# Performance work log

Hardware: AMD Instinct MI355X
Metric: run time of the kernel (lower is better)

## Reference

```python
import jax, jax.numpy as jnp
import numpy as np

B, S, D = 2, 2048, 2048
H, G = 32, 8            # n_heads, n_kv_groups
HD = D // H             # head_dim = 64
GS = H // G             # group_size = 4


def _rope(t, cos, sin):
    # t: (B, h, S, HD); cos/sin: (S, HD), start_pos = 0
    half = t.shape[-1] // 2
    rot = jnp.concatenate([-t[..., half:], t[..., :half]], axis=-1)
    return t * cos[None, None] + rot * sin[None, None]


def setup_inputs() -> dict:
    key = jax.random.key(0)
    ks = jax.random.split(key, 7)
    x = jax.random.normal(ks[0], (B, S, D), jnp.float32)
    cos = jax.random.normal(ks[1], (S, HD), jnp.float32)
    sin = jax.random.normal(ks[2], (S, HD), jnp.float32)
    mask = jnp.zeros((S, S), jnp.bool_)
    Wq = jax.random.normal(ks[3], (D, D), jnp.float32) * 0.02
    Wk = jax.random.normal(ks[4], (G * HD, D), jnp.float32) * 0.02
    Wv = jax.random.normal(ks[5], (G * HD, D), jnp.float32) * 0.02
    Wo = jax.random.normal(ks[6], (D, D), jnp.float32) * 0.02
    return {"x": x, "cos": cos, "sin": sin, "mask": mask,
            "Wq": Wq, "Wk": Wk, "Wv": Wv, "Wo": Wo}


def reference(x, cos, sin, mask, Wq, Wk, Wv, Wo):
    b, s, d = x.shape
    # projections (nn.Linear: y = x @ W.T)
    q = (x @ Wq.T).reshape(b, s, H, HD).transpose(0, 2, 1, 3)   # (b,H,s,HD)
    k = (x @ Wk.T).reshape(b, s, G, HD).transpose(0, 2, 1, 3)   # (b,G,s,HD)
    v = (x @ Wv.T).reshape(b, s, G, HD).transpose(0, 2, 1, 3)   # (b,G,s,HD)
    q = _rope(q, cos, sin)
    k = _rope(k, cos, sin)
    # GQA: heads grouped contiguously per kv group (equivalent to repeat_interleave on kv)
    qg = q.reshape(b, G, GS, s, HD)
    scores = jnp.einsum('bgmsd,bgtd->bgmst', qg, k) / jnp.sqrt(jnp.float32(HD))
    # NOTE: original calls non-inplace masked_fill and DISCARDS the result,
    # so the mask has no effect on the output; reproduced faithfully.
    attn = jax.nn.softmax(scores, axis=-1)
    y = jnp.einsum('bgmst,bgtd->bgmsd', attn, v)
    y = y.reshape(b, H, s, HD).transpose(0, 2, 1, 3).reshape(b, s, d)
    return y @ Wo.T
```

## Files before the change

### kernel.cpp

```cpp
#include <hip/hip_runtime.h>
#include <hip/hip_bf16.h>
#include <stdint.h>

#define B_ 2
#define S_ 2048
#define D_ 2048
#define H_ 32
#define G_ 8
#define HD_ 64
#define KVD (G_*HD_)

typedef unsigned short u16;
typedef unsigned int u32;
typedef __attribute__((ext_vector_type(8))) short s8v;
typedef __attribute__((ext_vector_type(4))) float f4v;
typedef __attribute__((ext_vector_type(4))) unsigned int u4v;

static __device__ __forceinline__ float bf2f(u16 u){ return __uint_as_float(((u32)u)<<16); }
static __device__ __forceinline__ u16 f2bf(float f){
  u32 b = __float_as_uint(f);
  return (u16)((b + 0x7FFFu + ((b>>16)&1u)) >> 16);
}
static __device__ __forceinline__ u32 pk2bf(float a, float b){
  float2 f2 = make_float2(a, b);
  __hip_bfloat162 h = __float22bfloat162_rn(f2);
  return *(u32*)&h;
}

struct CvtArgs {
  const float *x, *wq, *wk, *wv, *wo;
  u16 *xb, *wqkvb, *wob;
};
__global__ void k_cvt5(CvtArgs a){
  const int E0 = 2097152;
  const int E1 = E0 + 1048576;
  const int E2 = E1 + 262144;
  const int E3 = E2 + 262144;
  const int E4 = E3 + 1048576;
  int u = blockIdx.x*blockDim.x + threadIdx.x;
  int stride = gridDim.x*blockDim.x;
  for (; u < E4; u += stride){
    const float* s; u16* d; int off;
    if      (u < E0){ s = a.x;  d = a.xb;               off = u; }
    else if (u < E1){ s = a.wq; d = a.wqkvb;            off = u - E0; }
    else if (u < E2){ s = a.wk; d = a.wqkvb + 4194304;  off = u - E1; }
    else if (u < E3){ s = a.wv; d = a.wqkvb + 5242880;  off = u - E2; }
    else            { s = a.wo; d = a.wob;              off = u - E3; }
    float4 f = *(const float4*)(s + (long)off*4);
    uint2 o;
    o.x = (u32)f2bf(f.x) | ((u32)f2bf(f.y)<<16);
    o.y = (u32)f2bf(f.z) | ((u32)f2bf(f.w)<<16);
    *(uint2*)(d + (long)off*4) = o;
  }
}

template<int MODE>
__global__ __launch_bounds__(512) void k_gemm(const u16* __restrict__ A,
    const u16* __restrict__ Bw,
    void* __restrict__ C, void* __restrict__ C2, void* __restrict__ C3,
    const float* __restrict__ cs, const float* __restrict__ sn,
    int N_unused, int K){
  __shared__ u16 As[2][128*32];
  __shared__ u16 Bs[2][128*32];
  const int tid = threadIdx.x;
  const int lane = tid & 63, wid = tid >> 6;
  const int l15 = lane & 15, l4 = lane >> 4;
  const int wr = wid >> 1, wc = wid & 1;
  const long Arow0 = (long)blockIdx.x * 128;
  const long Brow0 = (long)blockIdx.y * 128;
  const int NKS = K >> 5;

  const int sc = tid;
  const int srow = sc >> 2, slot = sc & 3;
  const int ko = slot ^ (srow & 3);
  const u16* srcA0 = A  + (Arow0 + srow)*K + ko*8;
  const u16* srcB0 = Bw + (Brow0 + srow)*K + ko*8;
  auto stage = [&](int ks){
    int bsel = ks & 1, k0 = ks << 5;
    __builtin_amdgcn_global_load_lds(
        (__attribute__((address_space(1))) void*)(void*)(srcA0 + k0),
        (__attribute__((address_space(3))) void*)(&As[bsel][wid*512]), 16, 0, 0);
    __builtin_amdgcn_global_load_lds(
        (__attribute__((address_space(1))) void*)(void*)(srcB0 + k0),
        (__attribute__((address_space(3))) void*)(&Bs[bsel][wid*512]), 16, 0, 0);
  };

  f4v acc[2][4] = {};
  stage(0);
  for (int ks = 0; ks < NKS; ++ks){
    __syncthreads();
    if (ks + 1 < NKS) stage(ks + 1);
    const u16* AsB = As[ks & 1];
    const u16* BsB = Bs[ks & 1];
    s8v af[2], bf[4];
    #pragma unroll
    for (int m = 0; m < 2; ++m){
      int row = wr*32 + m*16 + l15;
      af[m] = *(const s8v*)((const char*)AsB + row*64 + ((l4 ^ (row & 3))<<4));
    }
    #pragma unroll
    for (int n = 0; n < 4; ++n){
      int col = wc*64 + n*16 + l15;
      bf[n] = *(const s8v*)((const char*)BsB + col*64 + ((l4 ^ (col & 3))<<4));
    }
    __builtin_amdgcn_s_setprio(1);
    #pragma unroll
    for (int m = 0; m < 2; ++m)
      #pragma unroll
      for (int n = 0; n < 4; ++n)
        acc[m][n] = __builtin_amdgcn_mfma_f32_16x16x32_bf16(af[m], bf[n], acc[m][n], 0, 0, 0);
    __builtin_amdgcn_s_setprio(0);
  }

  if (MODE == 0){
    #pragma unroll
    for (int m = 0; m < 2; ++m)
      #pragma unroll
      for (int n = 0; n < 4; ++n)
        #pragma unroll
        for (int i = 0; i < 4; ++i){
          long r = Arow0 + wr*32 + m*16 + l4*4 + i;
          long c = Brow0 + wc*64 + n*16 + l15;
          ((float*)C)[r*2048 + c] = acc[m][n][i];
        }
  } else {
    const long col0 = Brow0 + wc*64;
    if (col0 < 2560){
      u16* out; long cbase; int stride; float qs;
      if (col0 < 2048){ out = (u16*)C;  cbase = col0;        stride = 2048; qs = 0.125f*1.44269504f; }
      else            { out = (u16*)C2; cbase = col0 - 2048; stride = 512;  qs = 1.0f; }
      #pragma unroll
      for (int m = 0; m < 2; ++m){
        long r0 = Arow0 + wr*32 + m*16 + l4*4;
        #pragma unroll
        for (int i = 0; i < 4; ++i){
          int s = (int)((r0 + i) & (S_-1));
          const float* cb = cs + s*64 + l15;
          const float* sb = sn + s*64 + l15;
          #pragma unroll
          for (int n = 0; n < 2; ++n){
            float c0 = cb[n*16],      s0v = sb[n*16];
            float c1 = cb[n*16 + 32], s1v = sb[n*16 + 32];
            float t0 = acc[m][n][i], t1 = acc[m][n+2][i];
            long cA = cbase + n*16 + l15;
            out[(r0+i)*stride + cA]      = f2bf((t0*c0 - t1*s0v)*qs);
            out[(r0+i)*stride + cA + 32] = f2bf((t1*c1 + t0*s1v)*qs);
          }
        }
      }
    } else {
      u16* vt = (u16*)C3;
      int g = (int)((col0 - 2560) >> 6);
      #pragma unroll
      for (int m = 0; m < 2; ++m){
        long r0 = Arow0 + wr*32 + m*16 + l4*4;
        int b = (int)(r0 >> 11), s0 = (int)(r0 & (S_-1));
        #pragma unroll
        for (int n = 0; n < 4; ++n){
          int d = n*16 + l15;
          uint2 w;
          w.x = (u32)f2bf(acc[m][n][0]) | ((u32)f2bf(acc[m][n][1])<<16);
          w.y = (u32)f2bf(acc[m][n][2]) | ((u32)f2bf(acc[m][n][3])<<16);
          *(uint2*)(vt + ((long)(b*G_ + g)*64 + d)*S_ + s0) = w;
        }
      }
    }
  }
}

__global__ __launch_bounds__(512) void k_fattn(const u16* __restrict__ q,
    const u16* __restrict__ k, const u16* __restrict__ vt, u16* __restrict__ o){
  __shared__ u16 Ks[2][64*64];
  __shared__ u16 VTs[2][64*64];
  __shared__ u16 Ps[8][32*64];
  const int tid = threadIdx.x, lane = tid & 63, wid = tid >> 6;
  const int l15 = lane & 15, l4 = lane >> 4;
  const int qt = blockIdx.x, h = blockIdx.y, b = blockIdx.z;
  const int g = h >> 2;
  const long qrow0 = (long)b*S_ + qt*256 + wid*32;

  s8v aq[2][2];
  #pragma unroll
  for (int mf = 0; mf < 2; ++mf)
    #pragma unroll
    for (int kf = 0; kf < 2; ++kf)
      aq[mf][kf] = *(const s8v*)(q + (qrow0 + mf*16 + l15)*D_ + h*64 + kf*32 + l4*8);

  u4v ov; ov.x = ov.y = ov.z = ov.w = 0x3F803F80u;
  const s8v ones = *(s8v*)&ov;

  const int c = wid*64 + lane;
  const int srow = c >> 3, ko = (c & 7) ^ (srow & 7);
  const u16* ksrc0 = k  + ((long)b*S_ + srow)*KVD + g*64 + ko*8;
  const u16* vsrc0 = vt + ((long)(b*G_ + g)*64 + srow)*S_ + ko*8;

  auto stage = [&](int kt){
    int bsel = kt & 1;
    __builtin_amdgcn_global_load_lds(
        (__attribute__((address_space(1))) void*)(void*)(ksrc0 + (long)kt*64*KVD),
        (__attribute__((address_space(3))) void*)(&Ks[bsel][wid*512]), 16, 0, 0);
    __builtin_amdgcn_global_load_lds(
        (__attribute__((address_space(1))) void*)(void*)(vsrc0 + kt*64),
        (__attribute__((address_space(3))) void*)(&VTs[bsel][wid*512]), 16, 0, 0);
  };

  f4v oacc[2][4] = {};
  f4v lsacc[2] = {};

  stage(0);
  for (int kt = 0; kt < S_/64; ++kt){
    __syncthreads();
    if (kt + 1 < S_/64) stage(kt + 1);
    const u16* KsB = Ks[kt & 1];
    const u16* VsB = VTs[kt & 1];

    s8v bk[4][2];
    #pragma unroll
    for (int nf = 0; nf < 4; ++nf){
      int key = nf*16 + l15;
      #pragma unroll
      for (int kf = 0; kf < 2; ++kf)
        bk[nf][kf] = *(const s8v*)((const char*)KsB + key*128 + (((kf*4 + l4) ^ (key & 7))<<4));
    }
    f4v sacc[2][4] = {};
    __builtin_amdgcn_s_setprio(1);
    #pragma unroll
    for (int mf = 0; mf < 2; ++mf)
      #pragma unroll
      for (int nf = 0; nf < 4; ++nf)
        #pragma unroll
        for (int kf = 0; kf < 2; ++kf)
          sacc[mf][nf] = __builtin_amdgcn_mfma_f32_16x16x32_bf16(bk[nf][kf], aq[mf][kf], sacc[mf][nf], 0, 0, 0);
    __builtin_amdgcn_s_setprio(0);

    #pragma unroll
    for (int mf = 0; mf < 2; ++mf){
      int r = mf*16 + l15;
      char* pbase = (char*)Ps[wid] + r*128 + (l4 & 1)*8;
      #pragma unroll
      for (int nf = 0; nf < 4; ++nf){
        float p0 = __builtin_amdgcn_exp2f(sacc[mf][nf][0]);
        float p1 = __builtin_amdgcn_exp2f(sacc[mf][nf][1]);
        float p2 = __builtin_amdgcn_exp2f(sacc[mf][nf][2]);
        float p3 = __builtin_amdgcn_exp2f(sacc[mf][nf][3]);
        uint2 w; w.x = pk2bf(p0, p1); w.y = pk2bf(p2, p3);
        int slot = nf*2 + (l4 >> 1);
        *(uint2*)(pbase + ((slot ^ (r & 7))<<4)) = w;
      }
    }

    s8v ap[2][2];
    #pragma unroll
    for (int mf = 0; mf < 2; ++mf){
      int r = mf*16 + l15;
      #pragma unroll
      for (int kf = 0; kf < 2; ++kf)
        ap[mf][kf] = *(const s8v*)((const char*)Ps[wid] + r*128 + (((kf*4 + l4) ^ (r & 7))<<4));
    }
    __builtin_amdgcn_s_setprio(1);
    #pragma unroll
    for (int mf = 0; mf < 2; ++mf)
      #pragma unroll
      for (int kf = 0; kf < 2; ++kf)
        lsacc[mf] = __builtin_amdgcn_mfma_f32_16x16x32_bf16(ap[mf][kf], ones, lsacc[mf], 0, 0, 0);
    #pragma unroll
    for (int nd = 0; nd < 4; ++nd){
      int d = nd*16 + l15;
      #pragma unroll
      for (int kf = 0; kf < 2; ++kf){
        s8v bv = *(const s8v*)((const char*)VsB + d*128 + (((kf*4 + l4) ^ (d & 7))<<4));
        #pragma unroll
        for (int mf = 0; mf < 2; ++mf)
          oacc[mf][nd] = __builtin_amdgcn_mfma_f32_16x16x32_bf16(ap[mf][kf], bv, oacc[mf][nd], 0, 0, 0);
      }
    }
    __builtin_amdgcn_s_setprio(0);
  }

  #pragma unroll
  for (int mf = 0; mf < 2; ++mf){
    f4v li;
    #pragma unroll
    for (int i = 0; i < 4; ++i) li[i] = 1.f / lsacc[mf][i];
    #pragma unroll
    for (int nd = 0; nd < 4; ++nd){
      long r = qrow0 + mf*16 + l4*4;
      int cc = h*64 + nd*16 + l15;
      o[(r+0)*D_ + cc] = f2bf(oacc[mf][nd][0]*li[0]);
      o[(r+1)*D_ + cc] = f2bf(oacc[mf][nd][1]*li[1]);
      o[(r+2)*D_ + cc] = f2bf(oacc[mf][nd][2]*li[2]);
      o[(r+3)*D_ + cc] = f2bf(oacc[mf][nd][3]*li[3]);
    }
  }
}

extern "C" void kernel_launch(void* const* d_in, const int* in_sizes, int n_in,
                              void* d_out, int out_size, void* d_ws, size_t ws_size,
                              hipStream_t stream){
  const float* x    = (const float*)d_in[0];
  const float* cosp = (const float*)d_in[1];
  const float* sinp = (const float*)d_in[2];
  const float* Wq = (const float*)d_in[4];
  const float* Wk = (const float*)d_in[5];
  const float* Wv = (const float*)d_in[6];
  const float* Wo = (const float*)d_in[7];

  char* ws = (char*)d_ws;
  size_t off = 0;
  auto alloc = [&](size_t bytes)->char*{
    char* p = ws + off; off += (bytes + 255) & ~(size_t)255; return p;
  };
  u16* xb    = (u16*)alloc((size_t)8388608*2);
  u16* wqkvb = (u16*)alloc((size_t)6291456*2);
  u16* wob   = (u16*)alloc((size_t)4194304*2);
  u16* qb    = (u16*)alloc((size_t)8388608*2);
  u16* kb    = (u16*)alloc((size_t)2097152*2);
  u16* vtb   = (u16*)alloc((size_t)2097152*2);
  u16* ab    = (u16*)alloc((size_t)8388608*2);
  if (ws_size < off) return;

  CvtArgs ca{ x, Wq, Wk, Wv, Wo, xb, wqkvb, wob };
  k_cvt5<<<2048,256,0,stream>>>(ca);

  k_gemm<3><<<dim3(32,24,1),512,0,stream>>>(xb, wqkvb, qb, kb, vtb, cosp, sinp, 3072, 2048);

  k_fattn<<<dim3(8,32,2),512,0,stream>>>(qb, kb, vtb, ab);

  k_gemm<0><<<dim3(32,16,1),512,0,stream>>>(ab, wob, d_out, nullptr, nullptr, nullptr, nullptr, 2048, 2048);
}
```

Before: 206.9 us.

## Single-buffer K/V tiles in flash attention, raise occupancy, remap block order

```diff
diff --git a/kernel.cpp b/kernel.cpp
--- a/kernel.cpp
+++ b/kernel.cpp
@@ -168,14 +168,17 @@
   }
 }
 
-__global__ __launch_bounds__(512) void k_fattn(const u16* __restrict__ q,
+__global__ __launch_bounds__(512,6) void k_fattn(const u16* __restrict__ q,
     const u16* __restrict__ k, const u16* __restrict__ vt, u16* __restrict__ o){
-  __shared__ u16 Ks[2][64*64];
-  __shared__ u16 VTs[2][64*64];
+  __shared__ u16 Ks[64*64];
+  __shared__ u16 VTs[64*64];
   __shared__ u16 Ps[8][32*64];
   const int tid = threadIdx.x, lane = tid & 63, wid = tid >> 6;
   const int l15 = lane & 15, l4 = lane >> 4;
-  const int qt = blockIdx.x, h = blockIdx.y, b = blockIdx.z;
+  const int fid = blockIdx.x;
+  const int G = (fid >> 6)*8 + (fid & 7);
+  const int qt = (fid >> 3) & 7;
+  const int h = G & 31, b = G >> 5;
   const int g = h >> 2;
   const long qrow0 = (long)b*S_ + qt*256 + wid*32;
 
@@ -194,25 +197,17 @@
   const u16* ksrc0 = k  + ((long)b*S_ + srow)*KVD + g*64 + ko*8;
   const u16* vsrc0 = vt + ((long)(b*G_ + g)*64 + srow)*S_ + ko*8;
 
-  auto stage = [&](int kt){
-    int bsel = kt & 1;
+  f4v oacc[2][4] = {};
+  f4v lsacc[2] = {};
+
+  for (int kt = 0; kt < S_/64; ++kt){
     __builtin_amdgcn_global_load_lds(
         (__attribute__((address_space(1))) void*)(void*)(ksrc0 + (long)kt*64*KVD),
-        (__attribute__((address_space(3))) void*)(&Ks[bsel][wid*512]), 16, 0, 0);
+        (__attribute__((address_space(3))) void*)(&Ks[wid*512]), 16, 0, 0);
     __builtin_amdgcn_global_load_lds(
         (__attribute__((address_space(1))) void*)(void*)(vsrc0 + kt*64),
-        (__attribute__((address_space(3))) void*)(&VTs[bsel][wid*512]), 16, 0, 0);
-  };
-
-  f4v oacc[2][4] = {};
-  f4v lsacc[2] = {};
-
-  stage(0);
-  for (int kt = 0; kt < S_/64; ++kt){
+        (__attribute__((address_space(3))) void*)(&VTs[wid*512]), 16, 0, 0);
     __syncthreads();
-    if (kt + 1 < S_/64) stage(kt + 1);
-    const u16* KsB = Ks[kt & 1];
-    const u16* VsB = VTs[kt & 1];
 
     s8v bk[4][2];
     #pragma unroll
@@ -220,7 +215,7 @@
       int key = nf*16 + l15;
       #pragma unroll
       for (int kf = 0; kf < 2; ++kf)
-        bk[nf][kf] = *(const s8v*)((const char*)KsB + key*128 + (((kf*4 + l4) ^ (key & 7))<<4));
+        bk[nf][kf] = *(const s8v*)((const char*)Ks + key*128 + (((kf*4 + l4) ^ (key & 7))<<4));
     }
     f4v sacc[2][4] = {};
     __builtin_amdgcn_s_setprio(1);
@@ -257,24 +252,29 @@
       for (int kf = 0; kf < 2; ++kf)
         ap[mf][kf] = *(const s8v*)((const char*)Ps[wid] + r*128 + (((kf*4 + l4) ^ (r & 7))<<4));
     }
-    __builtin_amdgcn_s_setprio(1);
-    #pragma unroll
-    for (int mf = 0; mf < 2; ++mf)
-      #pragma unroll
-      for (int kf = 0; kf < 2; ++kf)
-        lsacc[mf] = __builtin_amdgcn_mfma_f32_16x16x32_bf16(ap[mf][kf], ones, lsacc[mf], 0, 0, 0);
+    s8v bv[4][2];
     #pragma unroll
     for (int nd = 0; nd < 4; ++nd){
       int d = nd*16 + l15;
       #pragma unroll
-      for (int kf = 0; kf < 2; ++kf){
-        s8v bv = *(const s8v*)((const char*)VsB + d*128 + (((kf*4 + l4) ^ (d & 7))<<4));
+      for (int kf = 0; kf < 2; ++kf)
+        bv[nd][kf] = *(const s8v*)((const char*)VTs + d*128 + (((kf*4 + l4) ^ (d & 7))<<4));
+    }
+    __builtin_amdgcn_s_setprio(1);
+    #pragma unroll
+    for (int mf = 0; mf < 2; ++mf)
+      #pragma unroll
+      for (int kf = 0; kf < 2; ++kf)
+        lsacc[mf] = __builtin_amdgcn_mfma_f32_16x16x32_bf16(ap[mf][kf], ones, lsacc[mf], 0, 0, 0);
+    #pragma unroll
+    for (int nd = 0; nd < 4; ++nd)
+      #pragma unroll
+      for (int kf = 0; kf < 2; ++kf)
         #pragma unroll
         for (int mf = 0; mf < 2; ++mf)
-          oacc[mf][nd] = __builtin_amdgcn_mfma_f32_16x16x32_bf16(ap[mf][kf], bv, oacc[mf][nd], 0, 0, 0);
-      }
-    }
+          oacc[mf][nd] = __builtin_amdgcn_mfma_f32_16x16x32_bf16(ap[mf][kf], bv[nd][kf], oacc[mf][nd], 0, 0, 0);
     __builtin_amdgcn_s_setprio(0);
+    __syncthreads();
   }
 
   #pragma unroll
@@ -324,7 +324,7 @@
 
   k_gemm<3><<<dim3(32,24,1),512,0,stream>>>(xb, wqkvb, qb, kb, vtb, cosp, sinp, 3072, 2048);
 
-  k_fattn<<<dim3(8,32,2),512,0,stream>>>(qb, kb, vtb, ab);
+  k_fattn<<<dim3(512,1,1),512,0,stream>>>(qb, kb, vtb, ab);
 
   k_gemm<0><<<dim3(32,16,1),512,0,stream>>>(ab, wob, d_out, nullptr, nullptr, nullptr, nullptr, 2048, 2048);
 }
```

Measured after the change: 510.0 us. 2.47x slower.
